# Performance work log

Hardware: AMD Instinct MI355X
Metric: run time of the kernel (lower is better)

## Reference

```python
import jax, jax.numpy as jnp
import numpy as np

B, T, CODE_NUM, MED_NUM = 256, 32, 4880, 1000
CODE_SIZE, H, OUT = 128, 128, 4880


def setup_inputs() -> dict:
    key = jax.random.key(0)
    ks = jax.random.split(key, 16)
    code_x = (jax.random.uniform(ks[0], (B, T, CODE_NUM)) < 0.05).astype(jnp.float32)
    medicine_codes = (jax.random.uniform(ks[1], (B, T, MED_NUM)) < 0.02).astype(jnp.float32)
    divided = (jax.random.uniform(ks[2], (B, T, CODE_NUM)) < 0.05).astype(jnp.float32)
    neighbors = (jax.random.uniform(ks[3], (B, T, CODE_NUM)) < 0.05).astype(jnp.float32)
    lens = jax.random.randint(ks[4], (B,), 1, T + 1)
    s = lambda fan: 1.0 / np.sqrt(fan)
    c_emb = jax.random.normal(ks[5], (CODE_NUM, CODE_SIZE)) * s(CODE_SIZE)
    m_emb = jax.random.normal(ks[6], (MED_NUM, CODE_SIZE)) * s(CODE_SIZE)
    W_c = jax.random.normal(ks[7], (CODE_SIZE, H)) * s(CODE_SIZE)
    W_m = jax.random.normal(ks[8], (CODE_SIZE, H)) * s(CODE_SIZE)
    Wa = jax.random.normal(ks[9], (3 * H, 32)) * s(3 * H)
    ba = jnp.zeros((32,), jnp.float32)
    va = jax.random.normal(ks[10], (32,)) * s(32)
    W_cls = jax.random.normal(ks[11], (3 * H, OUT)) * s(3 * H)
    b_cls = jnp.zeros((OUT,), jnp.float32)
    return dict(code_x=code_x, divided=divided, neighbors=neighbors, lens=lens,
                medicine_codes=medicine_codes, c_emb=c_emb, m_emb=m_emb,
                W_c=W_c, W_m=W_m, Wa=Wa, ba=ba, va=va, W_cls=W_cls, b_cls=b_cls)


def _forward(code_x, medicine_codes, lens, c_emb, m_emb, W_c, W_m, Wa, ba, va, W_cls, b_cls):
    # hypergraph_part: transform code/med embeddings, aggregate active codes per visit
    Hc = jnp.tanh(c_emb @ W_c)                      # [code_num, H]
    Hm = jnp.tanh(m_emb @ W_m)                      # [med_num, H]
    sum_c = jnp.einsum('btc,ch->bth', code_x, Hc)   # masked sum over active dx codes
    sum_m = jnp.einsum('btm,mh->bth', medicine_codes, Hm)
    h_c = sum_c / jnp.clip(code_x.sum(-1, keepdims=True), 1.0, None)
    h_m = sum_m / jnp.clip(medicine_codes.sum(-1, keepdims=True), 1.0, None)
    repre = jnp.concatenate([h_c, h_m, h_c * h_m], axis=-1)  # [B,T,3H]
    # DotProductAttention over visits, masked by lens
    scores = jnp.einsum('btk,k->bt', jnp.tanh(repre @ Wa + ba), va)
    mask = jnp.arange(T)[None, :] < lens[:, None]
    attn = jax.nn.softmax(jnp.where(mask, scores, -1e9), axis=-1)
    ctx = jnp.einsum('bt,btd->bd', attn, repre)     # [B,3H]
    # Classifier (dropout=identity in eval) + sigmoid
    return jax.nn.sigmoid(ctx @ W_cls + b_cls)      # [B,OUT]


def reference(code_x, divided, neighbors, lens, medicine_codes, c_emb, m_emb,
              W_c, W_m, Wa, ba, va, W_cls, b_cls):
    # divided/neighbors feed the transition branch whose output is unused
    # in the original forward's final prediction path.
    return _forward(code_x, medicine_codes, lens, c_emb, m_emb,
                    W_c, W_m, Wa, ba, va, W_cls, b_cls)
```

## Files before the change

kernel.cpp:

```cpp
#include <hip/hip_runtime.h>
#include <hip/hip_bf16.h>
#include <math.h>

#define Bsz 256
#define Tn 32
#define CODEN 4880
#define MEDN 1000
#define Hdim 128
#define OUTN 4880
#define R3H 384
#define KC_PAD 4896
#define KM_PAD 1024
#define NSC 153
#define NSM 32

typedef unsigned short u16;
typedef __attribute__((ext_vector_type(4))) float f32x4;
typedef __attribute__((ext_vector_type(8))) short s16x8;
typedef __attribute__((ext_vector_type(4))) unsigned int u32x4;

union PKU { u32x4 u; s16x8 s; };

__device__ inline unsigned f2bf(float f) {
  unsigned u = __float_as_uint(f);
  return (u + 0x7fffu + ((u >> 16) & 1u)) >> 16;
}
__device__ inline unsigned pack2(float f0, float f1) {
  return (__float_as_uint(f0) >> 16) | (__float_as_uint(f1) & 0xffff0000u);
}

__global__ __launch_bounds__(128) void k_emb(
    const float* __restrict__ c_emb, const float* __restrict__ m_emb,
    const float* __restrict__ W_c, const float* __restrict__ W_m,
    u16* __restrict__ HcT, u16* __restrict__ HmT) {
  int blk = blockIdx.x, h = threadIdx.x;
  bool is_med = blk >= KC_PAD;
  int c = is_med ? blk - KC_PAD : blk;
  int n = is_med ? MEDN : CODEN;
  u16* dst = is_med ? (HmT + (size_t)h * KM_PAD + c) : (HcT + (size_t)h * KC_PAD + c);
  if (c >= n) { *dst = 0; return; }
  const float* emb = (is_med ? m_emb : c_emb) + (size_t)c * Hdim;
  const float* W = is_med ? W_m : W_c;
  __shared__ float e[Hdim];
  e[h] = emb[h];
  __syncthreads();
  float acc = 0.f;
#pragma unroll 8
  for (int k = 0; k < Hdim; ++k) acc += e[k] * W[k * Hdim + h];
  *dst = (u16)f2bf(tanhf(acc));
}

__device__ inline void stageB(const u16* __restrict__ Bt, int k0, int ldk,
                              u16* buf, int ttid) {
#pragma unroll
  for (int it = 0; it < 4; ++it) {
    int c = it * 128 + ttid;
    const u16* src = Bt + (size_t)(c & 127) * ldk + k0 + (c >> 7) * 8;
#if __has_builtin(__builtin_amdgcn_global_load_lds)
    __builtin_amdgcn_global_load_lds(
        (const __attribute__((address_space(1))) void*)src,
        (__attribute__((address_space(3))) void*)(buf + c * 8), 16, 0, 0);
#else
    *(u32x4*)(buf + c * 8) = *(const u32x4*)src;
#endif
  }
}

__device__ inline void loadA(const float* __restrict__ Arow, int kb, int kmax,
                             float4& a0, float4& a1) {
  if (kb < kmax) {
    a0 = *(const float4*)(Arow + kb);
    a1 = *(const float4*)(Arow + kb + 4);
  } else {
    a0 = make_float4(0.f, 0.f, 0.f, 0.f);
    a1 = a0;
  }
}

__global__ __launch_bounds__(256, 1) void k_agg(
    const float* __restrict__ code_x, const float* __restrict__ med,
    const u16* __restrict__ HcT, const u16* __restrict__ HmT,
    const float* __restrict__ Wa, const float* __restrict__ ba,
    const float* __restrict__ va, const int* __restrict__ lens,
    float* __restrict__ ctx) {
  __shared__ u16 Bc[2][4096];
  __shared__ u16 Bm[2][4096];
  __shared__ float Wa_s[R3H * 32];
  __shared__ float rep_s[Tn][R3H + 4];
  __shared__ float sc_s[Tn];
  __shared__ float at_s[Tn];

  int b = blockIdx.x;
  int tid = threadIdx.x;
  int l = tid & 63;
  int l15 = l & 15, sub = l >> 4;
  bool codes_team = tid < 128;
  int ttid = codes_team ? tid : tid - 128;
  int twid = ttid >> 6;
  int trow = twid * 16 + l15;

  {
    const float4* s4 = (const float4*)Wa;
    float4* d4 = (float4*)Wa_s;
    for (int i = tid; i < R3H * 32 / 4; i += 256) d4[i] = s4[i];
  }

  f32x4 acc[8];
#pragma unroll
  for (int f = 0; f < 8; ++f) acc[f] = (f32x4){0.f, 0.f, 0.f, 0.f};
  float cnt = 0.f;

  const float* Arow;
  const u16* Bt;
  u16 *buf0, *buf1;
  int NS, kmax, ldk;
  if (codes_team) {
    Arow = code_x + (size_t)(b * Tn + trow) * CODEN;
    Bt = HcT; buf0 = Bc[0]; buf1 = Bc[1]; NS = NSC; kmax = CODEN; ldk = KC_PAD;
  } else {
    Arow = med + (size_t)(b * Tn + trow) * MEDN;
    Bt = HmT; buf0 = Bm[0]; buf1 = Bm[1]; NS = NSM; kmax = MEDN; ldk = KM_PAD;
  }

  float4 a0, a1;
  float4 n0 = make_float4(0.f, 0.f, 0.f, 0.f), n1 = n0;
  stageB(Bt, 0, ldk, buf0, ttid);
  loadA(Arow, sub * 8, kmax, a0, a1);

  for (int s = 0; s < NSC; ++s) {
    __syncthreads();
    bool active = s < NS;
    bool nxt = (s + 1) < NS;
    if (nxt) {
      stageB(Bt, (s + 1) * 32, ldk, ((s + 1) & 1) ? buf1 : buf0, ttid);
      loadA(Arow, (s + 1) * 32 + sub * 8, kmax, n0, n1);
    }
    if (active) {
      cnt += a0.x + a0.y + a0.z + a0.w + a1.x + a1.y + a1.z + a1.w;
      PKU pa;
      pa.u[0] = pack2(a0.x, a0.y);
      pa.u[1] = pack2(a0.z, a0.w);
      pa.u[2] = pack2(a1.x, a1.y);
      pa.u[3] = pack2(a1.z, a1.w);
      const u16* bb = ((s & 1) ? buf1 : buf0) + sub * 1024;
#pragma unroll
      for (int f = 0; f < 8; ++f) {
        PKU pb;
        pb.u = *(const u32x4*)(bb + (f * 16 + l15) * 8);
        acc[f] = __builtin_amdgcn_mfma_f32_16x16x32_bf16(pa.s, pb.s, acc[f], 0, 0, 0);
      }
      a0 = n0; a1 = n1;
    }
  }

  cnt += __shfl_xor(cnt, 16, 64);
  cnt += __shfl_xor(cnt, 32, 64);

  int cbase = codes_team ? 0 : 128;
#pragma unroll
  for (int j = 0; j < 4; ++j) {
    int r = sub * 4 + j;
    float cr = __shfl(cnt, r, 64);
    float iv = 1.0f / fmaxf(cr, 1.0f);
    int t = twid * 16 + r;
#pragma unroll
    for (int f = 0; f < 8; ++f)
      rep_s[t][cbase + f * 16 + l15] = acc[f][j] * iv;
  }
  __syncthreads();

  for (int i = tid; i < Tn * 128; i += 256) {
    int t = i >> 7, c = i & 127;
    rep_s[t][256 + c] = rep_s[t][c] * rep_s[t][128 + c];
  }
  __syncthreads();

  {
    int t = tid >> 3, j0 = (tid & 7) * 4;
    float u0 = 0.f, u1 = 0.f, u2 = 0.f, u3 = 0.f;
    for (int k = 0; k < R3H; ++k) {
      float r = rep_s[t][k];
      u0 += r * Wa_s[k * 32 + j0];
      u1 += r * Wa_s[k * 32 + j0 + 1];
      u2 += r * Wa_s[k * 32 + j0 + 2];
      u3 += r * Wa_s[k * 32 + j0 + 3];
    }
    float sv = tanhf(u0 + ba[j0])     * va[j0]
             + tanhf(u1 + ba[j0 + 1]) * va[j0 + 1]
             + tanhf(u2 + ba[j0 + 2]) * va[j0 + 2]
             + tanhf(u3 + ba[j0 + 3]) * va[j0 + 3];
    sv += __shfl_xor(sv, 1, 64);
    sv += __shfl_xor(sv, 2, 64);
    sv += __shfl_xor(sv, 4, 64);
    if ((tid & 7) == 0) sc_s[t] = sv;
  }
  __syncthreads();

  if (tid < Tn) {
    int len = lens[b];
    float s = sc_s[tid];
    bool valid = tid < len;
    float sm = valid ? s : -1e30f;
    float m = sm;
#pragma unroll
    for (int off = 16; off >= 1; off >>= 1) m = fmaxf(m, __shfl_xor(m, off, 32));
    float e = valid ? expf(sm - m) : 0.f;
    float su = e;
#pragma unroll
    for (int off = 16; off >= 1; off >>= 1) su += __shfl_xor(su, off, 32);
    at_s[tid] = e / su;
  }
  __syncthreads();

  for (int d = tid; d < R3H; d += 256) {
    float a = 0.f;
#pragma unroll
    for (int t = 0; t < Tn; ++t) a += at_s[t] * rep_s[t][d];
    ctx[(size_t)b * R3H + d] = a;
  }
}

__device__ inline void fma4(float4& a, float s, const float4& w) {
  a.x += s * w.x; a.y += s * w.y; a.z += s * w.z; a.w += s * w.w;
}

__global__ __launch_bounds__(256) void k_cls(
    const float* __restrict__ ctx, const float* __restrict__ W_cls,
    const float* __restrict__ b_cls, float* __restrict__ out) {
  __shared__ float cs_t[R3H * 8];
  int tid = threadIdx.x;
  int ob = blockIdx.x % 5;
  int b0 = (blockIdx.x / 5) * 8;
  for (int i = tid; i < R3H * 8; i += 256) {
    int k = i >> 3, r = i & 7;
    cs_t[i] = ctx[(size_t)(b0 + r) * R3H + k];
  }
  __syncthreads();
  int o0 = ob * 1024 + tid * 4;
  if (o0 >= OUTN) return;
  float4 acc[8];
#pragma unroll
  for (int r = 0; r < 8; ++r) acc[r] = make_float4(0.f, 0.f, 0.f, 0.f);
  const float* wp = W_cls + o0;
  for (int k = 0; k < R3H; k += 8) {
    float4 wv[8];
#pragma unroll
    for (int u = 0; u < 8; ++u) wv[u] = *(const float4*)(wp + (size_t)(k + u) * OUTN);
#pragma unroll
    for (int u = 0; u < 8; ++u) {
      float4 cA = *(const float4*)&cs_t[(k + u) * 8];
      float4 cB = *(const float4*)&cs_t[(k + u) * 8 + 4];
      fma4(acc[0], cA.x, wv[u]); fma4(acc[1], cA.y, wv[u]);
      fma4(acc[2], cA.z, wv[u]); fma4(acc[3], cA.w, wv[u]);
      fma4(acc[4], cB.x, wv[u]); fma4(acc[5], cB.y, wv[u]);
      fma4(acc[6], cB.z, wv[u]); fma4(acc[7], cB.w, wv[u]);
    }
  }
  float4 bc = *(const float4*)(b_cls + o0);
#pragma unroll
  for (int r = 0; r < 8; ++r) {
    float4 v;
    v.x = 1.f / (1.f + expf(-(acc[r].x + bc.x)));
    v.y = 1.f / (1.f + expf(-(acc[r].y + bc.y)));
    v.z = 1.f / (1.f + expf(-(acc[r].z + bc.z)));
    v.w = 1.f / (1.f + expf(-(acc[r].w + bc.w)));
    *(float4*)(out + (size_t)(b0 + r) * OUTN + o0) = v;
  }
}

extern "C" void kernel_launch(void* const* d_in, const int* in_sizes, int n_in,
                              void* d_out, int out_size, void* d_ws, size_t ws_size,
                              hipStream_t stream) {
  const float* code_x = (const float*)d_in[0];
  const int*   lens   = (const int*)d_in[3];
  const float* med    = (const float*)d_in[4];
  const float* c_emb  = (const float*)d_in[5];
  const float* m_emb  = (const float*)d_in[6];
  const float* W_c    = (const float*)d_in[7];
  const float* W_m    = (const float*)d_in[8];
  const float* Wa     = (const float*)d_in[9];
  const float* ba     = (const float*)d_in[10];
  const float* va     = (const float*)d_in[11];
  const float* W_cls  = (const float*)d_in[12];
  const float* b_cls  = (const float*)d_in[13];
  float* out = (float*)d_out;

  u16* HcT   = (u16*)d_ws;
  u16* HmT   = HcT + (size_t)128 * KC_PAD;
  float* ctx = (float*)(HmT + (size_t)128 * KM_PAD);

  hipLaunchKernelGGL(k_emb, dim3(KC_PAD + KM_PAD), dim3(128), 0, stream,
                     c_emb, m_emb, W_c, W_m, HcT, HmT);
  hipLaunchKernelGGL(k_agg, dim3(Bsz), dim3(256), 0, stream,
                     code_x, med, HcT, HmT, Wa, ba, va, lens, ctx);
  hipLaunchKernelGGL(k_cls, dim3(160), dim3(256), 0, stream,
                     ctx, W_cls, b_cls, out);
}
```

Measured before the change: 642.7 us.

## Split aggregation into a wide multi-block GEMM and a separate attention kernel

Moves the one-block-per-batch aggregation kernel to a 1024-block GEMM. Each block handles 16 visit rows of one batch for either codes or medicines, with four waves each owning 32 output columns. K per stage doubles to 64, and code padding grows to 4928 to match. Normalized code and medicine sums go to a global repre buffer, and a new k_post kernel computes the product term, attention scores, softmax and context per batch. The aim is more CUDs busy and more memory-level parallelism on the large multi-hot reads, at the cost of an extra launch, a global round trip for repre, and short medicine blocks imbalanced against code blocks.

```diff
diff --git a/kernel.cpp b/kernel.cpp
--- a/kernel.cpp
+++ b/kernel.cpp
@@ -9,10 +9,11 @@
 #define Hdim 128
 #define OUTN 4880
 #define R3H 384
-#define KC_PAD 4896
+#define RSTR 256
+#define KC_PAD 4928
 #define KM_PAD 1024
-#define NSC 153
-#define NSM 32
+#define NSC 77
+#define NSM 16
 
 typedef unsigned short u16;
 typedef __attribute__((ext_vector_type(4))) float f32x4;
@@ -51,10 +52,10 @@
 }
 
 __device__ inline void stageB(const u16* __restrict__ Bt, int k0, int ldk,
-                              u16* buf, int ttid) {
+                              u16* __restrict__ buf, int tid) {
 #pragma unroll
   for (int it = 0; it < 4; ++it) {
-    int c = it * 128 + ttid;
+    int c = it * 256 + tid;
     const u16* src = Bt + (size_t)(c & 127) * ldk + k0 + (c >> 7) * 8;
 #if __has_builtin(__builtin_amdgcn_global_load_lds)
     __builtin_amdgcn_global_load_lds(
@@ -66,124 +67,111 @@
   }
 }
 
-__device__ inline void loadA(const float* __restrict__ Arow, int kb, int kmax,
-                             float4& a0, float4& a1) {
-  if (kb < kmax) {
-    a0 = *(const float4*)(Arow + kb);
-    a1 = *(const float4*)(Arow + kb + 4);
-  } else {
-    a0 = make_float4(0.f, 0.f, 0.f, 0.f);
-    a1 = a0;
-  }
-}
-
-__global__ __launch_bounds__(256, 1) void k_agg(
+__device__ inline void loadA(const float* __restrict__ Arow, int k0, int kmax,
+                             float4* A) {
+  int kb = k0;
+  A[0] = (kb +  4 <= kmax) ? *(const float4*)(Arow + kb)      : make_float4(0,0,0,0);
+  A[1] = (kb +  8 <= kmax) ? *(const float4*)(Arow + kb + 4)  : make_float4(0,0,0,0);
+  A[2] = (kb + 36 <= kmax) ? *(const float4*)(Arow + kb + 32) : make_float4(0,0,0,0);
+  A[3] = (kb + 40 <= kmax) ? *(const float4*)(Arow + kb + 36) : make_float4(0,0,0,0);
+}
+
+__global__ __launch_bounds__(256, 4) void k_gemm(
     const float* __restrict__ code_x, const float* __restrict__ med,
     const u16* __restrict__ HcT, const u16* __restrict__ HmT,
-    const float* __restrict__ Wa, const float* __restrict__ ba,
-    const float* __restrict__ va, const int* __restrict__ lens,
-    float* __restrict__ ctx) {
-  __shared__ u16 Bc[2][4096];
-  __shared__ u16 Bm[2][4096];
-  __shared__ float Wa_s[R3H * 32];
-  __shared__ float rep_s[Tn][R3H + 4];
-  __shared__ float sc_s[Tn];
-  __shared__ float at_s[Tn];
-
-  int b = blockIdx.x;
+    float* __restrict__ repre) {
+  __shared__ u16 Bb[2][8192];
+  int gid = blockIdx.x;
+  bool is_med = gid >= 512;
+  int sg = is_med ? gid - 512 : gid;
+  int b = sg >> 1, half = sg & 1;
   int tid = threadIdx.x;
-  int l = tid & 63;
+  int w = tid >> 6, l = tid & 63;
   int l15 = l & 15, sub = l >> 4;
-  bool codes_team = tid < 128;
-  int ttid = codes_team ? tid : tid - 128;
-  int twid = ttid >> 6;
-  int trow = twid * 16 + l15;
-
-  {
-    const float4* s4 = (const float4*)Wa;
-    float4* d4 = (float4*)Wa_s;
-    for (int i = tid; i < R3H * 32 / 4; i += 256) d4[i] = s4[i];
-  }
-
-  f32x4 acc[8];
-#pragma unroll
-  for (int f = 0; f < 8; ++f) acc[f] = (f32x4){0.f, 0.f, 0.f, 0.f};
+  int row_g = b * Tn + half * 16 + l15;
+
+  const float* Arow; const u16* Bt; int NS, kmax, ldk, cbase;
+  if (is_med) { Arow = med    + (size_t)row_g * MEDN;  Bt = HmT; NS = NSM; kmax = MEDN;  ldk = KM_PAD; cbase = 128; }
+  else        { Arow = code_x + (size_t)row_g * CODEN; Bt = HcT; NS = NSC; kmax = CODEN; ldk = KC_PAD; cbase = 0; }
+
+  f32x4 acc[2] = {{0.f,0.f,0.f,0.f},{0.f,0.f,0.f,0.f}};
   float cnt = 0.f;
-
-  const float* Arow;
-  const u16* Bt;
-  u16 *buf0, *buf1;
-  int NS, kmax, ldk;
-  if (codes_team) {
-    Arow = code_x + (size_t)(b * Tn + trow) * CODEN;
-    Bt = HcT; buf0 = Bc[0]; buf1 = Bc[1]; NS = NSC; kmax = CODEN; ldk = KC_PAD;
-  } else {
-    Arow = med + (size_t)(b * Tn + trow) * MEDN;
-    Bt = HmT; buf0 = Bm[0]; buf1 = Bm[1]; NS = NSM; kmax = MEDN; ldk = KM_PAD;
-  }
-
-  float4 a0, a1;
-  float4 n0 = make_float4(0.f, 0.f, 0.f, 0.f), n1 = n0;
-  stageB(Bt, 0, ldk, buf0, ttid);
-  loadA(Arow, sub * 8, kmax, a0, a1);
-
-  for (int s = 0; s < NSC; ++s) {
+  float4 A[4], nA[4];
+
+  stageB(Bt, 0, ldk, Bb[0], tid);
+  loadA(Arow, sub * 8, kmax, A);
+
+  for (int s = 0; s < NS; ++s) {
     __syncthreads();
-    bool active = s < NS;
-    bool nxt = (s + 1) < NS;
-    if (nxt) {
-      stageB(Bt, (s + 1) * 32, ldk, ((s + 1) & 1) ? buf1 : buf0, ttid);
-      loadA(Arow, (s + 1) * 32 + sub * 8, kmax, n0, n1);
-    }
-    if (active) {
-      cnt += a0.x + a0.y + a0.z + a0.w + a1.x + a1.y + a1.z + a1.w;
-      PKU pa;
-      pa.u[0] = pack2(a0.x, a0.y);
-      pa.u[1] = pack2(a0.z, a0.w);
-      pa.u[2] = pack2(a1.x, a1.y);
-      pa.u[3] = pack2(a1.z, a1.w);
-      const u16* bb = ((s & 1) ? buf1 : buf0) + sub * 1024;
-#pragma unroll
-      for (int f = 0; f < 8; ++f) {
-        PKU pb;
-        pb.u = *(const u32x4*)(bb + (f * 16 + l15) * 8);
-        acc[f] = __builtin_amdgcn_mfma_f32_16x16x32_bf16(pa.s, pb.s, acc[f], 0, 0, 0);
-      }
-      a0 = n0; a1 = n1;
-    }
+    int cur = s & 1;
+    if (s + 1 < NS) {
+      stageB(Bt, (s + 1) * 64, ldk, Bb[cur ^ 1], tid);
+      loadA(Arow, (s + 1) * 64 + sub * 8, kmax, nA);
+    }
+    PKU pa0, pa1;
+    pa0.u[0] = pack2(A[0].x, A[0].y); pa0.u[1] = pack2(A[0].z, A[0].w);
+    pa0.u[2] = pack2(A[1].x, A[1].y); pa0.u[3] = pack2(A[1].z, A[1].w);
+    pa1.u[0] = pack2(A[2].x, A[2].y); pa1.u[1] = pack2(A[2].z, A[2].w);
+    pa1.u[2] = pack2(A[3].x, A[3].y); pa1.u[3] = pack2(A[3].z, A[3].w);
+#pragma unroll
+    for (int q = 0; q < 4; ++q)
+      cnt += A[q].x + A[q].y + A[q].z + A[q].w;
+    const u16* bbuf = Bb[cur];
+#pragma unroll
+    for (int f = 0; f < 2; ++f) {
+      int col = (w * 2 + f) * 16 + l15;
+      PKU pb0, pb1;
+      pb0.u = *(const u32x4*)(bbuf + ((size_t)(0 * 4 + sub) * 128 + col) * 8);
+      pb1.u = *(const u32x4*)(bbuf + ((size_t)(1 * 4 + sub) * 128 + col) * 8);
+      acc[f] = __builtin_amdgcn_mfma_f32_16x16x32_bf16(pa0.s, pb0.s, acc[f], 0, 0, 0);
+      acc[f] = __builtin_amdgcn_mfma_f32_16x16x32_bf16(pa1.s, pb1.s, acc[f], 0, 0, 0);
+    }
+#pragma unroll
+    for (int q = 0; q < 4; ++q) A[q] = nA[q];
   }
 
   cnt += __shfl_xor(cnt, 16, 64);
   cnt += __shfl_xor(cnt, 32, 64);
 
-  int cbase = codes_team ? 0 : 128;
 #pragma unroll
   for (int j = 0; j < 4; ++j) {
     int r = sub * 4 + j;
     float cr = __shfl(cnt, r, 64);
     float iv = 1.0f / fmaxf(cr, 1.0f);
-    int t = twid * 16 + r;
-#pragma unroll
-    for (int f = 0; f < 8; ++f)
-      rep_s[t][cbase + f * 16 + l15] = acc[f][j] * iv;
-  }
-  __syncthreads();
-
+    size_t rbase = (size_t)(b * Tn + half * 16 + r) * RSTR + cbase;
+#pragma unroll
+    for (int f = 0; f < 2; ++f)
+      repre[rbase + (w * 2 + f) * 16 + l15] = acc[f][j] * iv;
+  }
+}
+
+__global__ __launch_bounds__(256) void k_post(
+    const float* __restrict__ repre, const float* __restrict__ Wa,
+    const float* __restrict__ ba, const float* __restrict__ va,
+    const int* __restrict__ lens, float* __restrict__ ctx) {
+  __shared__ float rep_s[Tn][R3H + 4];
+  __shared__ float sc_s[Tn];
+  __shared__ float at_s[Tn];
+  int b = blockIdx.x, tid = threadIdx.x;
+
+  for (int i = tid; i < Tn * (RSTR / 4); i += 256) {
+    int t = i >> 6, c4 = i & 63;
+    f32x4 v = *(const f32x4*)(repre + (size_t)(b * Tn + t) * RSTR + c4 * 4);
+    *(f32x4*)&rep_s[t][c4 * 4] = v;
+  }
+  __syncthreads();
   for (int i = tid; i < Tn * 128; i += 256) {
     int t = i >> 7, c = i & 127;
     rep_s[t][256 + c] = rep_s[t][c] * rep_s[t][128 + c];
   }
   __syncthreads();
-
   {
     int t = tid >> 3, j0 = (tid & 7) * 4;
     float u0 = 0.f, u1 = 0.f, u2 = 0.f, u3 = 0.f;
     for (int k = 0; k < R3H; ++k) {
       float r = rep_s[t][k];
-      u0 += r * Wa_s[k * 32 + j0];
-      u1 += r * Wa_s[k * 32 + j0 + 1];
-      u2 += r * Wa_s[k * 32 + j0 + 2];
-      u3 += r * Wa_s[k * 32 + j0 + 3];
+      float4 wv = *(const float4*)(Wa + k * 32 + j0);
+      u0 += r * wv.x; u1 += r * wv.y; u2 += r * wv.z; u3 += r * wv.w;
     }
     float sv = tanhf(u0 + ba[j0])     * va[j0]
              + tanhf(u1 + ba[j0 + 1]) * va[j0 + 1]
@@ -195,7 +183,6 @@
     if ((tid & 7) == 0) sc_s[t] = sv;
   }
   __syncthreads();
-
   if (tid < Tn) {
     int len = lens[b];
     float s = sc_s[tid];
@@ -211,7 +198,6 @@
     at_s[tid] = e / su;
   }
   __syncthreads();
-
   for (int d = tid; d < R3H; d += 256) {
     float a = 0.f;
 #pragma unroll
@@ -285,14 +271,17 @@
   const float* b_cls  = (const float*)d_in[13];
   float* out = (float*)d_out;
 
-  u16* HcT   = (u16*)d_ws;
-  u16* HmT   = HcT + (size_t)128 * KC_PAD;
-  float* ctx = (float*)(HmT + (size_t)128 * KM_PAD);
+  u16* HcT = (u16*)d_ws;
+  u16* HmT = HcT + (size_t)128 * KC_PAD;
+  float* repre = (float*)(HmT + (size_t)128 * KM_PAD);
+  float* ctx = repre + (size_t)Bsz * Tn * RSTR;
 
   hipLaunchKernelGGL(k_emb, dim3(KC_PAD + KM_PAD), dim3(128), 0, stream,
                      c_emb, m_emb, W_c, W_m, HcT, HmT);
-  hipLaunchKernelGGL(k_agg, dim3(Bsz), dim3(256), 0, stream,
-                     code_x, med, HcT, HmT, Wa, ba, va, lens, ctx);
+  hipLaunchKernelGGL(k_gemm, dim3(1024), dim3(256), 0, stream,
+                     code_x, med, HcT, HmT, repre);
+  hipLaunchKernelGGL(k_post, dim3(Bsz), dim3(256), 0, stream,
+                     repre, Wa, ba, va, lens, ctx);
   hipLaunchKernelGGL(k_cls, dim3(160), dim3(256), 0, stream,
                      ctx, W_cls, b_cls, out);
 }
```

Result: faster. 609.6 us (-5.1%).
